# Optimization experiments

Measured on AMD Instinct MI355X. Metric: run time of the kernel, lower is better.

## Reference

```python
import jax, jax.numpy as jnp
import numpy as np

T = 5          # temporal_window_size
B = 512        # batch (graphs per timestep)
NA = 16        # num_agents (nodes per graph)
S = 64         # num_belief_states
A = 16         # action_dim
HID = 64       # hidden_dim per head
H = 4          # num_attn_heads
FD = HID * H   # 256, feature_dim
LAT = 128      # latent_dim
N = B * NA     # total nodes per timestep
FIN = S + A    # node feature dim
NEG_SLOPE = 0.2


def _edge_index():
    i, j = np.meshgrid(np.arange(NA), np.arange(NA), indexing='ij')
    m = i != j
    src_l, dst_l = i[m], j[m]                      # 240 intra-clique edges
    off = (np.arange(B) * NA)[:, None]
    src = (src_l[None] + off).ravel()
    dst = (dst_l[None] + off).ravel()
    loops = np.arange(N)                           # PyG GATConv add_self_loops=True
    src = np.concatenate([src, loops])
    dst = np.concatenate([dst, loops])
    return jnp.asarray(np.stack([src, dst]), dtype=jnp.int64)


def setup_inputs() -> dict:
    key = jax.random.key(0)
    ks = jax.random.split(key, 24)
    xav = lambda k, shp: jax.random.normal(k, shp, jnp.float32) * np.float32(np.sqrt(2.0 / (shp[0] + shp[-1])))
    return {
        'signals': jax.random.normal(ks[0], (T, B, S), jnp.float32),
        'neighbor_actions': jax.random.normal(ks[1], (T, B, NA * A), jnp.float32),
        'lin_w0': xav(ks[2], (FD, FIN)),
        'att_src0': xav(ks[3], (H, HID)),
        'att_dst0': xav(ks[4], (H, HID)),
        'bias0': jnp.zeros((FD,), jnp.float32),
        'lin_w1': xav(ks[5], (FD, FD)),
        'att_src1': xav(ks[6], (H, HID)),
        'att_dst1': xav(ks[7], (H, HID)),
        'bias1': jnp.zeros((FD,), jnp.float32),
        'in_proj_w': xav(ks[8], (3 * FD, FD)),
        'in_proj_b': jnp.zeros((3 * FD,), jnp.float32),
        'out_proj_w': xav(ks[9], (FD, FD)),
        'out_proj_b': jnp.zeros((FD,), jnp.float32),
        'w_mean': xav(ks[10], (LAT, FD)),
        'b_mean': jnp.zeros((LAT,), jnp.float32),
        'w_logvar': xav(ks[11], (LAT, FD)),
        'b_logvar': jnp.zeros((LAT,), jnp.float32),
        'w_belief': xav(ks[12], (S, FD)),
        'b_belief': jnp.zeros((S,), jnp.float32),
        'edge_index': _edge_index(),
    }


def _segment_softmax(e, seg, num_segments):
    # e: [E, T, H]; softmax over edges sharing the same target node.
    m = jax.ops.segment_max(e, seg, num_segments=num_segments)
    e = jnp.exp(e - m[seg])
    s = jax.ops.segment_sum(e, seg, num_segments=num_segments)
    return e / s[seg]


def _gat(x, src, dst, w, a_src, a_dst, b):
    # x: [N, T, Fin] -> [N, T, H*HID]   (PyG GATConv, concat heads)
    xl = jnp.einsum('ntf,of->nto', x, w).reshape(N, T, H, HID)
    e_src = jnp.einsum('nthc,hc->nth', xl, a_src)[src]   # [E, T, H]
    e_dst = jnp.einsum('nthc,hc->nth', xl, a_dst)[dst]
    e = jax.nn.leaky_relu(e_src + e_dst, NEG_SLOPE)
    alpha = _segment_softmax(e, dst, N)                  # per-target softmax
    out = jax.ops.segment_sum(alpha[..., None] * xl[src], dst, num_segments=N)
    return out.reshape(N, T, FD) + b


def reference(signals, neighbor_actions, lin_w0, att_src0, att_dst0, bias0,
              lin_w1, att_src1, att_dst1, bias1, in_proj_w, in_proj_b,
              out_proj_w, out_proj_b, w_mean, b_mean, w_logvar, b_logvar,
              w_belief, b_belief, edge_index):
    # --- _construct_graph (vectorized over time window + batch) ---
    acts = neighbor_actions.reshape(T, B, NA, A)
    beliefs = jnp.zeros((T, B, NA, S), signals.dtype).at[:, :, 0, :].set(signals)
    nodes = jnp.concatenate([beliefs, acts], -1).reshape(T, N, FIN)
    nodes = jnp.transpose(nodes, (1, 0, 2))              # [N, T, FIN]
    src, dst = edge_index[0], edge_index[1]
    x = jax.nn.relu(_gat(nodes, src, dst, lin_w0, att_src0, att_dst0, bias0))
    x = jax.nn.relu(_gat(x, src, dst, lin_w1, att_src1, att_dst1, bias1))
    # --- ego-node sequence: nodes 0, NA, 2*NA, ... ---
    seq = x[::NA]                                        # [B, T, FD]
    # --- temporal MultiheadAttention (batch_first, eval) ---
    qkv = seq @ in_proj_w.T + in_proj_b
    q, k, v = jnp.split(qkv, 3, axis=-1)
    dh = FD // H
    q = q.reshape(B, T, H, dh); k = k.reshape(B, T, H, dh); v = v.reshape(B, T, H, dh)
    scores = jnp.einsum('bqhd,bkhd->bhqk', q, k) / jnp.sqrt(jnp.asarray(dh, seq.dtype))
    # torch float attn_mask is ADDITIVE: mask[i,j]=1 if j<=i else 0
    mask = (jnp.arange(T)[:, None] >= jnp.arange(T)[None, :]).astype(seq.dtype)
    attn = jax.nn.softmax(scores + mask[None, None], axis=-1)
    ctx = jnp.einsum('bhqk,bkhd->bqhd', attn, v).reshape(B, T, FD)
    ctx = ctx @ out_proj_w.T + out_proj_b
    feat = ctx[:, -1]                                    # [B, FD]
    # --- heads ---
    mean = feat @ w_mean.T + b_mean
    logvar = feat @ w_logvar.T + b_logvar
    belief = jax.nn.softmax(feat @ w_belief.T + b_belief, axis=-1)
    return (mean, logvar, belief)
```

## Files before the change

### kernel.cpp

```cpp
#include <hip/hip_runtime.h>
#include <hip/hip_bf16.h>


__device__ __forceinline__ float wave_sum64(float v) {
    #pragma unroll
    for (int off = 32; off > 0; off >>= 1) v += __shfl_xor(v, off, 64);
    return v;
}
__device__ __forceinline__ float wave_max64(float v) {
    #pragma unroll
    for (int off = 32; off > 0; off >>= 1) v = fmaxf(v, __shfl_xor(v, off, 64));
    return v;
}

__global__ __launch_bounds__(256) void k_pre(
    const float* __restrict__ w0, const float* __restrict__ w1,
    const float* __restrict__ wip, const float* __restrict__ wop,
    const float* __restrict__ wm, const float* __restrict__ wlv,
    const float* __restrict__ wb,
    const float* __restrict__ as0, const float* __restrict__ ad0,
    const float* __restrict__ as1, const float* __restrict__ ad1,
    float* __restrict__ tws,
    float* __restrict__ u1, float* __restrict__ ud1,
    float* __restrict__ pa0, float* __restrict__ pd0)
{
    const int tid = threadIdx.x;
    if (blockIdx.x < 1680) {
        int i = blockIdx.x * 256 + tid;
        float v;
        if (i < 16384) {
            int k = i >> 8, n = i & 255;
            v = w0[n * 80 + k];
        } else if (i < 20480) {
            int j = i - 16384; int k = j >> 8, n = j & 255;
            v = w0[n * 80 + 64 + k];
        } else if (i < 86016) {
            int j = i - 20480; int k = j >> 8, n = j & 255;
            v = w1[n * 256 + k];
        } else if (i < 282624) {
            int j = i - 86016; int k = j / 768, n = j - k * 768;
            v = wip[n * 256 + k];
        } else if (i < 348160) {
            int j = i - 282624; int k = j >> 8, n = j & 255;
            v = wop[n * 256 + k];
        } else {
            int j = i - 348160; int k = j / 320, o = j - k * 320;
            if (o < 128)      v = wm[o * 256 + k];
            else if (o < 256) v = wlv[(o - 128) * 256 + k];
            else              v = wb[(o - 256) * 256 + k];
        }
        tws[i] = v;
        return;
    }
    for (int q = 0; q < 4; q++) {
        int idx = q * 256 + tid;
        int h = idx >> 8, k = idx & 255;
        float su = 0.f, sd = 0.f;
        for (int c = 0; c < 64; c++) {
            float wv = w1[(h * 64 + c) * 256 + k];
            su = fmaf(as1[h * 64 + c], wv, su);
            sd = fmaf(ad1[h * 64 + c], wv, sd);
        }
        u1[idx] = su; ud1[idx] = sd;
    }
    if (tid < 64) {
        int h = tid >> 4, k = tid & 15;
        float su = 0.f, sd = 0.f;
        for (int c = 0; c < 64; c++) {
            float wv = w0[(h * 64 + c) * 80 + 64 + k];
            su = fmaf(as0[h * 64 + c], wv, su);
            sd = fmaf(ad0[h * 64 + c], wv, sd);
        }
        pa0[tid] = su; pd0[tid] = sd;
    }
}

__global__ __launch_bounds__(256) void k_gat(
    const float* __restrict__ sig,
    const float* __restrict__ nact,
    const float* __restrict__ W0sT,
    const float* __restrict__ W0aT,
    const float* __restrict__ W1T,
    const float* __restrict__ u1g, const float* __restrict__ ud1g,
    const float* __restrict__ pa0g, const float* __restrict__ pd0g,
    const float* __restrict__ as0, const float* __restrict__ ad0,
    const float* __restrict__ b0, const float* __restrict__ b1,
    float* __restrict__ seqf)
{
    __shared__ float sigL[5][64];
    __shared__ float actL[5][16][16];
    __shared__ float SL[5][258];
    __shared__ float u1L[4][256], ud1L[4][256];
    __shared__ float pa0L[64], pd0L[64];
    __shared__ float sSL[5][4], dSL[5][4];
    __shared__ float es0L[5][16][4], ed0L[5][16][4];
    __shared__ float a0g[4][16][16];
    __shared__ float dL[4][16][16];
    __shared__ float x1L[16][258];
    __shared__ float espL[16][4][4];
    __shared__ float edpL[4][4];
    __shared__ float es1L[16][4];
    __shared__ float edL[4];
    __shared__ float alpha1L[4][16];
    __shared__ float zL[5][4][258];

    const int tid = threadIdx.x;
    const int b = blockIdx.x;

    for (int i = tid; i < 320; i += 256)
        sigL[i >> 6][i & 63] = sig[((i >> 6) * 512 + b) * 64 + (i & 63)];
    for (int i = tid; i < 1280; i += 256) {
        int g = i >> 8, r = i & 255;
        actL[g][r >> 4][r & 15] = nact[(g * 512 + b) * 256 + r];
    }
    for (int q = 0; q < 4; q++) {
        int idx = q * 256 + tid;
        u1L[idx >> 8][idx & 255] = u1g[idx];
        ud1L[idx >> 8][idx & 255] = ud1g[idx];
    }
    if (tid < 64) { pa0L[tid] = pa0g[tid]; pd0L[tid] = pd0g[tid]; }
    __syncthreads();

    {
        const int n = tid;
        float acc[5] = {0, 0, 0, 0, 0};
        for (int k = 0; k < 64; k++) {
            float wv = W0sT[k * 256 + n];
            #pragma unroll
            for (int g = 0; g < 5; g++) acc[g] = fmaf(sigL[g][k], wv, acc[g]);
        }
        #pragma unroll
        for (int g = 0; g < 5; g++) SL[g][n] = acc[g];
    }
    __syncthreads();

    if (tid < 20) {
        int g = tid / 4, h = tid & 3;
        float su = 0.f, sd = 0.f;
        for (int c = 0; c < 64; c++) {
            float sv = SL[g][h * 64 + c];
            su = fmaf(sv, as0[h * 64 + c], su);
            sd = fmaf(sv, ad0[h * 64 + c], sd);
        }
        sSL[g][h] = su; dSL[g][h] = sd;
    }
    __syncthreads();

    for (int q = tid; q < 320; q += 256) {
        int g = q >> 6, r = q & 63, m = r >> 2, h = r & 3;
        float su = (m == 0) ? sSL[g][h] : 0.f;
        float sd = (m == 0) ? dSL[g][h] : 0.f;
        #pragma unroll
        for (int k = 0; k < 16; k++) {
            float av = actL[g][m][k];
            su = fmaf(av, pa0L[h * 16 + k], su);
            sd = fmaf(av, pd0L[h * 16 + k], sd);
        }
        es0L[g][m][h] = su; ed0L[g][m][h] = sd;
    }
    __syncthreads();

    for (int g = 0; g < 5; g++) {
        if (tid < 64) {
            int h = tid >> 4, j = tid & 15;
            float ej = ed0L[g][j][h];
            float e[16], m = -1e30f;
            #pragma unroll
            for (int s = 0; s < 16; s++) {
                float x = es0L[g][s][h] + ej;
                x = (x >= 0.f) ? x : 0.2f * x;
                e[s] = x; m = fmaxf(m, x);
            }
            float sum = 0.f;
            #pragma unroll
            for (int s = 0; s < 16; s++) { e[s] = __expf(e[s] - m); sum += e[s]; }
            float inv = 1.f / sum;
            #pragma unroll
            for (int s = 0; s < 16; s++) a0g[h][j][s] = e[s] * inv;
        }
        __syncthreads();

        #pragma unroll
        for (int q = 0; q < 4; q++) {
            int idx = q * 256 + tid;
            int h = idx >> 8, j = (idx >> 4) & 15, k = idx & 15;
            float a = 0.f;
            #pragma unroll
            for (int s = 0; s < 16; s++)
                a = fmaf(a0g[h][j][s], actL[g][s][k], a);
            dL[h][j][k] = a;
        }
        __syncthreads();

        {
            const int n = tid, h = n >> 6;
            float sv = SL[g][n], b0v = b0[n];
            float accj[16];
            #pragma unroll
            for (int j = 0; j < 16; j++)
                accj[j] = fmaf(a0g[h][j][0], sv, b0v);
            #pragma unroll
            for (int k = 0; k < 16; k++) {
                float wv = W0aT[k * 256 + n];
                #pragma unroll
                for (int j = 0; j < 16; j++)
                    accj[j] = fmaf(dL[h][j][k], wv, accj[j]);
            }
            #pragma unroll
            for (int j = 0; j < 16; j++)
                x1L[j][n] = fmaxf(accj[j], 0.f);
        }
        __syncthreads();

        {
            int m = tid >> 4, h = (tid >> 2) & 3, p = tid & 3;
            float a = 0.f;
            for (int kk = 0; kk < 64; kk++) {
                int k = kk * 4 + p;
                a = fmaf(x1L[m][k], u1L[h][k], a);
            }
            espL[m][h][p] = a;
            if (m == 0) {
                float ad = 0.f;
                for (int kk = 0; kk < 64; kk++) {
                    int k = kk * 4 + p;
                    ad = fmaf(x1L[0][k], ud1L[h][k], ad);
                }
                edpL[h][p] = ad;
            }
        }
        __syncthreads();
        if (tid < 64) {
            int m = tid >> 2, h = tid & 3;
            es1L[m][h] = espL[m][h][0] + espL[m][h][1] + espL[m][h][2] + espL[m][h][3];
        }
        if (tid < 4)
            edL[tid] = edpL[tid][0] + edpL[tid][1] + edpL[tid][2] + edpL[tid][3];
        __syncthreads();

        if (tid < 4) {
            int h = tid;
            float ej = edL[h];
            float e[16], m = -1e30f;
            #pragma unroll
            for (int s = 0; s < 16; s++) {
                float x = es1L[s][h] + ej;
                x = (x >= 0.f) ? x : 0.2f * x;
                e[s] = x; m = fmaxf(m, x);
            }
            float sum = 0.f;
            #pragma unroll
            for (int s = 0; s < 16; s++) { e[s] = __expf(e[s] - m); sum += e[s]; }
            float inv = 1.f / sum;
            #pragma unroll
            for (int s = 0; s < 16; s++) alpha1L[h][s] = e[s] * inv;
        }
        __syncthreads();

        {
            const int k = tid;
            float xv[16];
            #pragma unroll
            for (int s = 0; s < 16; s++) xv[s] = x1L[s][k];
            #pragma unroll
            for (int h = 0; h < 4; h++) {
                float zv = 0.f;
                #pragma unroll
                for (int s = 0; s < 16; s++)
                    zv = fmaf(alpha1L[h][s], xv[s], zv);
                zL[g][h][k] = zv;
            }
        }
        __syncthreads();
    }

    {
        const int n = tid, h = n >> 6;
        float b1v = b1[n];
        float acc[5] = {b1v, b1v, b1v, b1v, b1v};
        for (int k = 0; k < 256; k++) {
            float wv = W1T[k * 256 + n];
            #pragma unroll
            for (int g = 0; g < 5; g++)
                acc[g] = fmaf(zL[g][h][k], wv, acc[g]);
        }
        #pragma unroll
        for (int g = 0; g < 5; g++)
            seqf[(b * 5 + g) * 256 + n] = fmaxf(acc[g], 0.f);
    }
}

__global__ __launch_bounds__(768) void k_stage2(
    const float* __restrict__ seqf,
    const float* __restrict__ wipT,
    const float* __restrict__ bip,
    const float* __restrict__ wopT,
    const float* __restrict__ bop,
    const float* __restrict__ whT,
    const float* __restrict__ bm, const float* __restrict__ blv,
    const float* __restrict__ bb,
    float* __restrict__ out)
{
    __shared__ float sseq[2][5][256];
    __shared__ float kL[2][5][256], vL[2][5][256], qL[2][256];
    __shared__ float ctxL[2][256], featL[2][256];
    __shared__ float beliefL[2][64];
    const int tid = threadIdx.x;
    const int b0 = blockIdx.x * 2;

    {
        float* sflat = &sseq[0][0][0];
        for (int i = tid; i < 2560; i += 768)
            sflat[i] = seqf[b0 * 1280 + i];
    }
    __syncthreads();

    {
        const int kind = tid >> 8, n = tid & 255;
        if (kind == 0) {
            float a0 = 0.f, a1 = 0.f;
            for (int k = 0; k < 256; k++) {
                float wv = wipT[k * 768 + n];
                a0 = fmaf(sseq[0][4][k], wv, a0);
                a1 = fmaf(sseq[1][4][k], wv, a1);
            }
            float bv = bip[n];
            qL[0][n] = a0 + bv; qL[1][n] = a1 + bv;
        } else {
            const float* wcol = wipT + kind * 256 + n;
            float acc[2][5];
            #pragma unroll
            for (int gb = 0; gb < 2; gb++)
                #pragma unroll
                for (int t = 0; t < 5; t++) acc[gb][t] = 0.f;
            for (int k = 0; k < 256; k++) {
                float wv = wcol[k * 768];
                #pragma unroll
                for (int gb = 0; gb < 2; gb++) {
                    #pragma unroll
                    for (int t = 0; t < 5; t++)
                        acc[gb][t] = fmaf(sseq[gb][t][k], wv, acc[gb][t]);
                }
            }
            float bv = bip[kind * 256 + n];
            float* dst = (kind == 1) ? &kL[0][0][0] : &vL[0][0][0];
            #pragma unroll
            for (int gb = 0; gb < 2; gb++)
                #pragma unroll
                for (int t = 0; t < 5; t++)
                    dst[gb * 1280 + t * 256 + n] = acc[gb][t] + bv;
        }
    }
    __syncthreads();

    if (tid < 512) {
        const int gb = tid >> 8, col = tid & 255;
        float q4 = qL[gb][col];
        float sc[5];
        #pragma unroll
        for (int t = 0; t < 5; t++)
            sc[t] = wave_sum64(q4 * kL[gb][t][col]) * 0.125f;
        float m = sc[0];
        #pragma unroll
        for (int t = 1; t < 5; t++) m = fmaxf(m, sc[t]);
        float p[5], sum = 0.f;
        #pragma unroll
        for (int t = 0; t < 5; t++) { p[t] = __expf(sc[t] - m); sum += p[t]; }
        float inv = 1.f / sum, cv = 0.f;
        #pragma unroll
        for (int t = 0; t < 5; t++) cv = fmaf(p[t], vL[gb][t][col], cv);
        ctxL[gb][col] = cv * inv;
    }
    __syncthreads();

    if (tid < 512) {
        const int gb = tid >> 8, n = tid & 255;
        float acc = 0.f;
        for (int k = 0; k < 256; k++)
            acc = fmaf(ctxL[gb][k], wopT[k * 256 + n], acc);
        featL[gb][n] = acc + bop[n];
    }
    __syncthreads();

    if (tid < 640) {
        const int gb = tid / 320, j = tid - gb * 320;
        float acc = 0.f;
        for (int k = 0; k < 256; k++)
            acc = fmaf(featL[gb][k], whT[k * 320 + j], acc);
        if (j < 128) {
            out[(b0 + gb) * 128 + j] = acc + bm[j];
        } else if (j < 256) {
            out[65536 + (b0 + gb) * 128 + (j - 128)] = acc + blv[j - 128];
        } else {
            beliefL[gb][j - 256] = acc + bb[j - 256];
        }
    }
    __syncthreads();

    if (tid < 128) {
        int gb = tid >> 6, lane = tid & 63;
        float lg = beliefL[gb][lane];
        float m = wave_max64(lg);
        float e = __expf(lg - m);
        float s = wave_sum64(e);
        out[131072 + (b0 + gb) * 64 + lane] = e / s;
    }
}

extern "C" void kernel_launch(void* const* d_in, const int* in_sizes, int n_in,
                              void* d_out, int out_size, void* d_ws, size_t ws_size,
                              hipStream_t stream) {
    const float* sig  = (const float*)d_in[0];
    const float* nact = (const float*)d_in[1];
    const float* w0   = (const float*)d_in[2];
    const float* as0  = (const float*)d_in[3];
    const float* ad0  = (const float*)d_in[4];
    const float* b0   = (const float*)d_in[5];
    const float* w1   = (const float*)d_in[6];
    const float* as1  = (const float*)d_in[7];
    const float* ad1  = (const float*)d_in[8];
    const float* b1   = (const float*)d_in[9];
    const float* wip  = (const float*)d_in[10];
    const float* bip  = (const float*)d_in[11];
    const float* wop  = (const float*)d_in[12];
    const float* bop  = (const float*)d_in[13];
    const float* wm   = (const float*)d_in[14];
    const float* bm   = (const float*)d_in[15];
    const float* wlv  = (const float*)d_in[16];
    const float* blv  = (const float*)d_in[17];
    const float* wb   = (const float*)d_in[18];
    const float* bb   = (const float*)d_in[19];

    float* ws    = (float*)d_ws;
    float* seqf  = ws;
    float* tws   = ws + 655360;
    float* W0sT  = tws;
    float* W0aT  = tws + 16384;
    float* W1T   = tws + 20480;
    float* wipT  = tws + 86016;
    float* wopT  = tws + 282624;
    float* whT   = tws + 348160;
    float* u1    = ws + 1085440;
    float* ud1   = ws + 1086464;
    float* pa0   = ws + 1087488;
    float* pd0   = ws + 1087552;

    k_pre   <<<1681, 256, 0, stream>>>(w0, w1, wip, wop, wm, wlv, wb,
                                       as0, ad0, as1, ad1,
                                       tws, u1, ud1, pa0, pd0);
    k_gat   <<<512, 256, 0, stream>>>(sig, nact, W0sT, W0aT, W1T,
                                      u1, ud1, pa0, pd0, as0, ad0, b0, b1, seqf);
    k_stage2<<<256, 768, 0, stream>>>(seqf, wipT, bip, wopT, bop, whT,
                                      bm, blv, bb, (float*)d_out);
}
```

Measured before the change: 205.2 us.

## Fuse GAT and temporal-attention stages into one kernel per graph

Merges the GAT kernel and the temporal attention/heads kernel into a single kernel, one block per graph, so the per-graph sequence features stay in shared memory instead of round-tripping through a global workspace. Shared memory is packed into one manually laid out buffer that reuses dead GAT regions for the q/k/v and context buffers, and the u1/ud1 rows are padded. This removes one launch and the seqf global write and read. In exchange, stage-2 weight reads are no longer shared across two graphs per block, and each block now streams the full QKV weight matrix alone with only 256 threads.

Result: slower. 211.7 us (+3.2%).

```diff
diff --git a/kernel.cpp b/kernel.cpp
--- a/kernel.cpp
+++ b/kernel.cpp
@@ -75,223 +75,15 @@
     }
 }
 
-__global__ __launch_bounds__(256) void k_gat(
+__global__ __launch_bounds__(256) void k_fused(
     const float* __restrict__ sig,
     const float* __restrict__ nact,
-    const float* __restrict__ W0sT,
-    const float* __restrict__ W0aT,
+    const float* __restrict__ W0sT, const float* __restrict__ W0aT,
     const float* __restrict__ W1T,
     const float* __restrict__ u1g, const float* __restrict__ ud1g,
     const float* __restrict__ pa0g, const float* __restrict__ pd0g,
     const float* __restrict__ as0, const float* __restrict__ ad0,
     const float* __restrict__ b0, const float* __restrict__ b1,
-    float* __restrict__ seqf)
-{
-    __shared__ float sigL[5][64];
-    __shared__ float actL[5][16][16];
-    __shared__ float SL[5][258];
-    __shared__ float u1L[4][256], ud1L[4][256];
-    __shared__ float pa0L[64], pd0L[64];
-    __shared__ float sSL[5][4], dSL[5][4];
-    __shared__ float es0L[5][16][4], ed0L[5][16][4];
-    __shared__ float a0g[4][16][16];
-    __shared__ float dL[4][16][16];
-    __shared__ float x1L[16][258];
-    __shared__ float espL[16][4][4];
-    __shared__ float edpL[4][4];
-    __shared__ float es1L[16][4];
-    __shared__ float edL[4];
-    __shared__ float alpha1L[4][16];
-    __shared__ float zL[5][4][258];
-
-    const int tid = threadIdx.x;
-    const int b = blockIdx.x;
-
-    for (int i = tid; i < 320; i += 256)
-        sigL[i >> 6][i & 63] = sig[((i >> 6) * 512 + b) * 64 + (i & 63)];
-    for (int i = tid; i < 1280; i += 256) {
-        int g = i >> 8, r = i & 255;
-        actL[g][r >> 4][r & 15] = nact[(g * 512 + b) * 256 + r];
-    }
-    for (int q = 0; q < 4; q++) {
-        int idx = q * 256 + tid;
-        u1L[idx >> 8][idx & 255] = u1g[idx];
-        ud1L[idx >> 8][idx & 255] = ud1g[idx];
-    }
-    if (tid < 64) { pa0L[tid] = pa0g[tid]; pd0L[tid] = pd0g[tid]; }
-    __syncthreads();
-
-    {
-        const int n = tid;
-        float acc[5] = {0, 0, 0, 0, 0};
-        for (int k = 0; k < 64; k++) {
-            float wv = W0sT[k * 256 + n];
-            #pragma unroll
-            for (int g = 0; g < 5; g++) acc[g] = fmaf(sigL[g][k], wv, acc[g]);
-        }
-        #pragma unroll
-        for (int g = 0; g < 5; g++) SL[g][n] = acc[g];
-    }
-    __syncthreads();
-
-    if (tid < 20) {
-        int g = tid / 4, h = tid & 3;
-        float su = 0.f, sd = 0.f;
-        for (int c = 0; c < 64; c++) {
-            float sv = SL[g][h * 64 + c];
-            su = fmaf(sv, as0[h * 64 + c], su);
-            sd = fmaf(sv, ad0[h * 64 + c], sd);
-        }
-        sSL[g][h] = su; dSL[g][h] = sd;
-    }
-    __syncthreads();
-
-    for (int q = tid; q < 320; q += 256) {
-        int g = q >> 6, r = q & 63, m = r >> 2, h = r & 3;
-        float su = (m == 0) ? sSL[g][h] : 0.f;
-        float sd = (m == 0) ? dSL[g][h] : 0.f;
-        #pragma unroll
-        for (int k = 0; k < 16; k++) {
-            float av = actL[g][m][k];
-            su = fmaf(av, pa0L[h * 16 + k], su);
-            sd = fmaf(av, pd0L[h * 16 + k], sd);
-        }
-        es0L[g][m][h] = su; ed0L[g][m][h] = sd;
-    }
-    __syncthreads();
-
-    for (int g = 0; g < 5; g++) {
-        if (tid < 64) {
-            int h = tid >> 4, j = tid & 15;
-            float ej = ed0L[g][j][h];
-            float e[16], m = -1e30f;
-            #pragma unroll
-            for (int s = 0; s < 16; s++) {
-                float x = es0L[g][s][h] + ej;
-                x = (x >= 0.f) ? x : 0.2f * x;
-                e[s] = x; m = fmaxf(m, x);
-            }
-            float sum = 0.f;
-            #pragma unroll
-            for (int s = 0; s < 16; s++) { e[s] = __expf(e[s] - m); sum += e[s]; }
-            float inv = 1.f / sum;
-            #pragma unroll
-            for (int s = 0; s < 16; s++) a0g[h][j][s] = e[s] * inv;
-        }
-        __syncthreads();
-
-        #pragma unroll
-        for (int q = 0; q < 4; q++) {
-            int idx = q * 256 + tid;
-            int h = idx >> 8, j = (idx >> 4) & 15, k = idx & 15;
-            float a = 0.f;
-            #pragma unroll
-            for (int s = 0; s < 16; s++)
-                a = fmaf(a0g[h][j][s], actL[g][s][k], a);
-            dL[h][j][k] = a;
-        }
-        __syncthreads();
-
-        {
-            const int n = tid, h = n >> 6;
-            float sv = SL[g][n], b0v = b0[n];
-            float accj[16];
-            #pragma unroll
-            for (int j = 0; j < 16; j++)
-                accj[j] = fmaf(a0g[h][j][0], sv, b0v);
-            #pragma unroll
-            for (int k = 0; k < 16; k++) {
-                float wv = W0aT[k * 256 + n];
-                #pragma unroll
-                for (int j = 0; j < 16; j++)
-                    accj[j] = fmaf(dL[h][j][k], wv, accj[j]);
-            }
-            #pragma unroll
-            for (int j = 0; j < 16; j++)
-                x1L[j][n] = fmaxf(accj[j], 0.f);
-        }
-        __syncthreads();
-
-        {
-            int m = tid >> 4, h = (tid >> 2) & 3, p = tid & 3;
-            float a = 0.f;
-            for (int kk = 0; kk < 64; kk++) {
-                int k = kk * 4 + p;
-                a = fmaf(x1L[m][k], u1L[h][k], a);
-            }
-            espL[m][h][p] = a;
-            if (m == 0) {
-                float ad = 0.f;
-                for (int kk = 0; kk < 64; kk++) {
-                    int k = kk * 4 + p;
-                    ad = fmaf(x1L[0][k], ud1L[h][k], ad);
-                }
-                edpL[h][p] = ad;
-            }
-        }
-        __syncthreads();
-        if (tid < 64) {
-            int m = tid >> 2, h = tid & 3;
-            es1L[m][h] = espL[m][h][0] + espL[m][h][1] + espL[m][h][2] + espL[m][h][3];
-        }
-        if (tid < 4)
-            edL[tid] = edpL[tid][0] + edpL[tid][1] + edpL[tid][2] + edpL[tid][3];
-        __syncthreads();
-
-        if (tid < 4) {
-            int h = tid;
-            float ej = edL[h];
-            float e[16], m = -1e30f;
-            #pragma unroll
-            for (int s = 0; s < 16; s++) {
-                float x = es1L[s][h] + ej;
-                x = (x >= 0.f) ? x : 0.2f * x;
-                e[s] = x; m = fmaxf(m, x);
-            }
-            float sum = 0.f;
-            #pragma unroll
-            for (int s = 0; s < 16; s++) { e[s] = __expf(e[s] - m); sum += e[s]; }
-            float inv = 1.f / sum;
-            #pragma unroll
-            for (int s = 0; s < 16; s++) alpha1L[h][s] = e[s] * inv;
-        }
-        __syncthreads();
-
-        {
-            const int k = tid;
-            float xv[16];
-            #pragma unroll
-            for (int s = 0; s < 16; s++) xv[s] = x1L[s][k];
-            #pragma unroll
-            for (int h = 0; h < 4; h++) {
-                float zv = 0.f;
-                #pragma unroll
-                for (int s = 0; s < 16; s++)
-                    zv = fmaf(alpha1L[h][s], xv[s], zv);
-                zL[g][h][k] = zv;
-            }
-        }
-        __syncthreads();
-    }
-
-    {
-        const int n = tid, h = n >> 6;
-        float b1v = b1[n];
-        float acc[5] = {b1v, b1v, b1v, b1v, b1v};
-        for (int k = 0; k < 256; k++) {
-            float wv = W1T[k * 256 + n];
-            #pragma unroll
-            for (int g = 0; g < 5; g++)
-                acc[g] = fmaf(zL[g][h][k], wv, acc[g]);
-        }
-        #pragma unroll
-        for (int g = 0; g < 5; g++)
-            seqf[(b * 5 + g) * 256 + n] = fmaxf(acc[g], 0.f);
-    }
-}
-
-__global__ __launch_bounds__(768) void k_stage2(
-    const float* __restrict__ seqf,
     const float* __restrict__ wipT,
     const float* __restrict__ bip,
     const float* __restrict__ wopT,
@@ -301,65 +93,254 @@
     const float* __restrict__ bb,
     float* __restrict__ out)
 {
-    __shared__ float sseq[2][5][256];
-    __shared__ float kL[2][5][256], vL[2][5][256], qL[2][256];
-    __shared__ float ctxL[2][256], featL[2][256];
-    __shared__ float beliefL[2][64];
+    __shared__ __align__(16) char smem[75232];
+    float* sigL   = (float*)(smem + 0);
+    float* actL   = (float*)(smem + 1280);
+    float* SL     = (float*)(smem + 6400);
+    float* u1L    = (float*)(smem + 11560);
+    float* ud1L   = (float*)(smem + 15720);
+    float* pa0L   = (float*)(smem + 19880);
+    float* pd0L   = (float*)(smem + 20136);
+    float* sSL    = (float*)(smem + 20392);
+    float* dSL    = (float*)(smem + 20472);
+    float* es0L   = (float*)(smem + 20552);
+    float* ed0L   = (float*)(smem + 21832);
+    float* a0g    = (float*)(smem + 23112);
+    float* dL     = (float*)(smem + 27208);
+    float* x1L    = (float*)(smem + 31304);
+    float* espL   = (float*)(smem + 47816);
+    float* edpL   = (float*)(smem + 48840);
+    float* es1L   = (float*)(smem + 48904);
+    float* edL    = (float*)(smem + 49160);
+    float* alpha1L= (float*)(smem + 49176);
+    float* zL     = (float*)(smem + 49432);
+    float* sseq   = (float*)(smem + 70072);
+    float* kLp    = (float*)(smem + 11560);
+    float* vLp    = (float*)(smem + 16680);
+    float* qLp    = (float*)(smem + 23112);
+    float* ctxLp  = (float*)(smem + 24136);
+    float* featLp = (float*)(smem + 25160);
+    float* belLp  = (float*)(smem + 27208);
+
     const int tid = threadIdx.x;
-    const int b0 = blockIdx.x * 2;
+    const int b = blockIdx.x;
+
+    for (int i = tid; i < 320; i += 256)
+        sigL[i] = sig[((i >> 6) * 512 + b) * 64 + (i & 63)];
+    for (int i = tid; i < 1280; i += 256)
+        actL[i] = nact[((i >> 8) * 512 + b) * 256 + (i & 255)];
+    #pragma unroll
+    for (int q = 0; q < 4; q++) {
+        int idx = q * 256 + tid;
+        int h = idx >> 8, k = idx & 255;
+        u1L[h * 260 + k] = u1g[idx];
+        ud1L[h * 260 + k] = ud1g[idx];
+    }
+    if (tid < 64) { pa0L[tid] = pa0g[tid]; pd0L[tid] = pd0g[tid]; }
+    __syncthreads();
 
     {
-        float* sflat = &sseq[0][0][0];
-        for (int i = tid; i < 2560; i += 768)
-            sflat[i] = seqf[b0 * 1280 + i];
-    }
-    __syncthreads();
+        const int n = tid;
+        float acc[5] = {0, 0, 0, 0, 0};
+        for (int k = 0; k < 64; k++) {
+            float wv = W0sT[k * 256 + n];
+            #pragma unroll
+            for (int g = 0; g < 5; g++) acc[g] = fmaf(sigL[g * 64 + k], wv, acc[g]);
+        }
+        #pragma unroll
+        for (int g = 0; g < 5; g++) SL[g * 258 + n] = acc[g];
+    }
+    __syncthreads();
+
+    if (tid < 20) {
+        int g = tid / 4, h = tid & 3;
+        float su = 0.f, sd = 0.f;
+        for (int c = 0; c < 64; c++) {
+            float sv = SL[g * 258 + h * 64 + c];
+            su = fmaf(sv, as0[h * 64 + c], su);
+            sd = fmaf(sv, ad0[h * 64 + c], sd);
+        }
+        sSL[g * 4 + h] = su; dSL[g * 4 + h] = sd;
+    }
+    __syncthreads();
+
+    for (int q = tid; q < 320; q += 256) {
+        int g = q >> 6, r = q & 63, m = r >> 2, h = r & 3;
+        float su = (m == 0) ? sSL[g * 4 + h] : 0.f;
+        float sd = (m == 0) ? dSL[g * 4 + h] : 0.f;
+        #pragma unroll
+        for (int k = 0; k < 16; k++) {
+            float av = actL[g * 256 + m * 16 + k];
+            su = fmaf(av, pa0L[h * 16 + k], su);
+            sd = fmaf(av, pd0L[h * 16 + k], sd);
+        }
+        es0L[g * 64 + m * 4 + h] = su; ed0L[g * 64 + m * 4 + h] = sd;
+    }
+    __syncthreads();
+
+    for (int g = 0; g < 5; g++) {
+        if (tid < 64) {
+            int h = tid >> 4, j = tid & 15;
+            float ej = ed0L[g * 64 + j * 4 + h];
+            float e[16], m = -1e30f;
+            #pragma unroll
+            for (int s = 0; s < 16; s++) {
+                float x = es0L[g * 64 + s * 4 + h] + ej;
+                x = (x >= 0.f) ? x : 0.2f * x;
+                e[s] = x; m = fmaxf(m, x);
+            }
+            float sum = 0.f;
+            #pragma unroll
+            for (int s = 0; s < 16; s++) { e[s] = __expf(e[s] - m); sum += e[s]; }
+            float inv = 1.f / sum;
+            #pragma unroll
+            for (int s = 0; s < 16; s++) a0g[h * 256 + j * 16 + s] = e[s] * inv;
+        }
+        __syncthreads();
+
+        #pragma unroll
+        for (int q = 0; q < 4; q++) {
+            int idx = q * 256 + tid;
+            int h = idx >> 8, j = (idx >> 4) & 15, k = idx & 15;
+            float a = 0.f;
+            #pragma unroll
+            for (int s = 0; s < 16; s++)
+                a = fmaf(a0g[h * 256 + j * 16 + s], actL[g * 256 + s * 16 + k], a);
+            dL[h * 256 + j * 16 + k] = a;
+        }
+        __syncthreads();
+
+        {
+            const int n = tid, h = n >> 6;
+            float sv = SL[g * 258 + n], b0v = b0[n];
+            float accj[16];
+            #pragma unroll
+            for (int j = 0; j < 16; j++)
+                accj[j] = fmaf(a0g[h * 256 + j * 16], sv, b0v);
+            #pragma unroll
+            for (int k = 0; k < 16; k++) {
+                float wv = W0aT[k * 256 + n];
+                #pragma unroll
+                for (int j = 0; j < 16; j++)
+                    accj[j] = fmaf(dL[h * 256 + j * 16 + k], wv, accj[j]);
+            }
+            #pragma unroll
+            for (int j = 0; j < 16; j++)
+                x1L[j * 258 + n] = fmaxf(accj[j], 0.f);
+        }
+        __syncthreads();
+
+        {
+            int m = tid >> 4, h = (tid >> 2) & 3, p = tid & 3;
+            float a = 0.f;
+            for (int kk = 0; kk < 64; kk++) {
+                int k = kk * 4 + p;
+                a = fmaf(x1L[m * 258 + k], u1L[h * 260 + k], a);
+            }
+            espL[m * 16 + h * 4 + p] = a;
+            if (m == 0) {
+                float ad = 0.f;
+                for (int kk = 0; kk < 64; kk++) {
+                    int k = kk * 4 + p;
+                    ad = fmaf(x1L[k], ud1L[h * 260 + k], ad);
+                }
+                edpL[h * 4 + p] = ad;
+            }
+        }
+        __syncthreads();
+        if (tid < 64) {
+            int m = tid >> 2, h = tid & 3;
+            const float* e = espL + m * 16 + h * 4;
+            es1L[m * 4 + h] = e[0] + e[1] + e[2] + e[3];
+        }
+        if (tid < 4)
+            edL[tid] = edpL[tid * 4] + edpL[tid * 4 + 1] + edpL[tid * 4 + 2] + edpL[tid * 4 + 3];
+        __syncthreads();
+
+        if (tid < 4) {
+            int h = tid;
+            float ej = edL[h];
+            float e[16], m = -1e30f;
+            #pragma unroll
+            for (int s = 0; s < 16; s++) {
+                float x = es1L[s * 4 + h] + ej;
+                x = (x >= 0.f) ? x : 0.2f * x;
+                e[s] = x; m = fmaxf(m, x);
+            }
+            float sum = 0.f;
+            #pragma unroll
+            for (int s = 0; s < 16; s++) { e[s] = __expf(e[s] - m); sum += e[s]; }
+            float inv = 1.f / sum;
+            #pragma unroll
+            for (int s = 0; s < 16; s++) alpha1L[h * 16 + s] = e[s] * inv;
+        }
+        __syncthreads();
+
+        {
+            const int k = tid;
+            float xv[16];
+            #pragma unroll
+            for (int s = 0; s < 16; s++) xv[s] = x1L[s * 258 + k];
+            #pragma unroll
+            for (int h = 0; h < 4; h++) {
+                float zv = 0.f;
+                #pragma unroll
+                for (int s = 0; s < 16; s++)
+                    zv = fmaf(alpha1L[h * 16 + s], xv[s], zv);
+                zL[g * 1032 + h * 258 + k] = zv;
+            }
+        }
+        __syncthreads();
+    }
 
     {
-        const int kind = tid >> 8, n = tid & 255;
-        if (kind == 0) {
-            float a0 = 0.f, a1 = 0.f;
-            for (int k = 0; k < 256; k++) {
-                float wv = wipT[k * 768 + n];
-                a0 = fmaf(sseq[0][4][k], wv, a0);
-                a1 = fmaf(sseq[1][4][k], wv, a1);
-            }
-            float bv = bip[n];
-            qL[0][n] = a0 + bv; qL[1][n] = a1 + bv;
-        } else {
-            const float* wcol = wipT + kind * 256 + n;
-            float acc[2][5];
-            #pragma unroll
-            for (int gb = 0; gb < 2; gb++)
-                #pragma unroll
-                for (int t = 0; t < 5; t++) acc[gb][t] = 0.f;
-            for (int k = 0; k < 256; k++) {
-                float wv = wcol[k * 768];
-                #pragma unroll
-                for (int gb = 0; gb < 2; gb++) {
-                    #pragma unroll
-                    for (int t = 0; t < 5; t++)
-                        acc[gb][t] = fmaf(sseq[gb][t][k], wv, acc[gb][t]);
-                }
-            }
-            float bv = bip[kind * 256 + n];
-            float* dst = (kind == 1) ? &kL[0][0][0] : &vL[0][0][0];
-            #pragma unroll
-            for (int gb = 0; gb < 2; gb++)
-                #pragma unroll
-                for (int t = 0; t < 5; t++)
-                    dst[gb * 1280 + t * 256 + n] = acc[gb][t] + bv;
-        }
-    }
-    __syncthreads();
-
-    if (tid < 512) {
-        const int gb = tid >> 8, col = tid & 255;
-        float q4 = qL[gb][col];
+        const int n = tid, h = n >> 6;
+        float b1v = b1[n];
+        float acc[5] = {b1v, b1v, b1v, b1v, b1v};
+        for (int k = 0; k < 256; k++) {
+            float wv = W1T[k * 256 + n];
+            #pragma unroll
+            for (int g = 0; g < 5; g++)
+                acc[g] = fmaf(zL[g * 1032 + h * 258 + k], wv, acc[g]);
+        }
+        #pragma unroll
+        for (int g = 0; g < 5; g++)
+            sseq[g * 258 + n] = fmaxf(acc[g], 0.f);
+    }
+    __syncthreads();
+
+    {
+        const int n = tid;
+        float accq = 0.f, acck[5] = {0, 0, 0, 0, 0}, accv[5] = {0, 0, 0, 0, 0};
+        for (int k = 0; k < 256; k++) {
+            float wq = wipT[k * 768 + n];
+            float wk = wipT[k * 768 + 256 + n];
+            float wv = wipT[k * 768 + 512 + n];
+            accq = fmaf(sseq[4 * 258 + k], wq, accq);
+            #pragma unroll
+            for (int t = 0; t < 5; t++) {
+                float sv = sseq[t * 258 + k];
+                acck[t] = fmaf(sv, wk, acck[t]);
+                accv[t] = fmaf(sv, wv, accv[t]);
+            }
+        }
+        qLp[n] = accq + bip[n];
+        float bk = bip[256 + n], bv = bip[512 + n];
+        #pragma unroll
+        for (int t = 0; t < 5; t++) {
+            kLp[t * 256 + n] = acck[t] + bk;
+            vLp[t * 256 + n] = accv[t] + bv;
+        }
+    }
+    __syncthreads();
+
+    {
+        const int col = tid;
+        float q4 = qLp[col];
         float sc[5];
         #pragma unroll
         for (int t = 0; t < 5; t++)
-            sc[t] = wave_sum64(q4 * kL[gb][t][col]) * 0.125f;
+            sc[t] = wave_sum64(q4 * kLp[t * 256 + col]) * 0.125f;
         float m = sc[0];
         #pragma unroll
         for (int t = 1; t < 5; t++) m = fmaxf(m, sc[t]);
@@ -368,42 +349,36 @@
         for (int t = 0; t < 5; t++) { p[t] = __expf(sc[t] - m); sum += p[t]; }
         float inv = 1.f / sum, cv = 0.f;
         #pragma unroll
-        for (int t = 0; t < 5; t++) cv = fmaf(p[t], vL[gb][t][col], cv);
-        ctxL[gb][col] = cv * inv;
-    }
-    __syncthreads();
-
-    if (tid < 512) {
-        const int gb = tid >> 8, n = tid & 255;
+        for (int t = 0; t < 5; t++) cv = fmaf(p[t], vLp[t * 256 + col], cv);
+        ctxLp[col] = cv * inv;
+    }
+    __syncthreads();
+
+    {
+        const int n = tid;
         float acc = 0.f;
         for (int k = 0; k < 256; k++)
-            acc = fmaf(ctxL[gb][k], wopT[k * 256 + n], acc);
-        featL[gb][n] = acc + bop[n];
-    }
-    __syncthreads();
-
-    if (tid < 640) {
-        const int gb = tid / 320, j = tid - gb * 320;
+            acc = fmaf(ctxLp[k], wopT[k * 256 + n], acc);
+        featLp[n] = acc + bop[n];
+    }
+    __syncthreads();
+
+    for (int j = tid; j < 320; j += 256) {
         float acc = 0.f;
         for (int k = 0; k < 256; k++)
-            acc = fmaf(featL[gb][k], whT[k * 320 + j], acc);
-        if (j < 128) {
-            out[(b0 + gb) * 128 + j] = acc + bm[j];
-        } else if (j < 256) {
-            out[65536 + (b0 + gb) * 128 + (j - 128)] = acc + blv[j - 128];
-        } else {
-            beliefL[gb][j - 256] = acc + bb[j - 256];
-        }
-    }
-    __syncthreads();
-
-    if (tid < 128) {
-        int gb = tid >> 6, lane = tid & 63;
-        float lg = beliefL[gb][lane];
+            acc = fmaf(featLp[k], whT[k * 320 + j], acc);
+        if (j < 128)       out[b * 128 + j] = acc + bm[j];
+        else if (j < 256)  out[65536 + b * 128 + (j - 128)] = acc + blv[j - 128];
+        else               belLp[j - 256] = acc + bb[j - 256];
+    }
+    __syncthreads();
+
+    if (tid < 64) {
+        float lg = belLp[tid];
         float m = wave_max64(lg);
         float e = __expf(lg - m);
         float s = wave_sum64(e);
-        out[131072 + (b0 + gb) * 64 + lane] = e / s;
+        out[131072 + b * 64 + tid] = e / s;
     }
 }
 
@@ -432,24 +407,23 @@
     const float* bb   = (const float*)d_in[19];
 
     float* ws    = (float*)d_ws;
-    float* seqf  = ws;
-    float* tws   = ws + 655360;
+    float* tws   = ws;
     float* W0sT  = tws;
     float* W0aT  = tws + 16384;
     float* W1T   = tws + 20480;
     float* wipT  = tws + 86016;
     float* wopT  = tws + 282624;
     float* whT   = tws + 348160;
-    float* u1    = ws + 1085440;
-    float* ud1   = ws + 1086464;
-    float* pa0   = ws + 1087488;
-    float* pd0   = ws + 1087552;
-
-    k_pre   <<<1681, 256, 0, stream>>>(w0, w1, wip, wop, wm, wlv, wb,
-                                       as0, ad0, as1, ad1,
-                                       tws, u1, ud1, pa0, pd0);
-    k_gat   <<<512, 256, 0, stream>>>(sig, nact, W0sT, W0aT, W1T,
-                                      u1, ud1, pa0, pd0, as0, ad0, b0, b1, seqf);
-    k_stage2<<<256, 768, 0, stream>>>(seqf, wipT, bip, wopT, bop, whT,
-                                      bm, blv, bb, (float*)d_out);
+    float* u1    = ws + 430080;
+    float* ud1   = ws + 431104;
+    float* pa0   = ws + 432128;
+    float* pd0   = ws + 432192;
+
+    k_pre  <<<1681, 256, 0, stream>>>(w0, w1, wip, wop, wm, wlv, wb,
+                                      as0, ad0, as1, ad1,
+                                      tws, u1, ud1, pa0, pd0);
+    k_fused<<<512, 256, 0, stream>>>(sig, nact, W0sT, W0aT, W1T,
+                                     u1, ud1, pa0, pd0, as0, ad0, b0, b1,
+                                     wipT, bip, wopT, bop, whT, bm, blv, bb,
+                                     (float*)d_out);
 }
```

## Split GAT kernel across timesteps: one block per (batch, timestep) pair

Applied to the files above, without the earlier changes.

The GAT kernel previously ran 512 blocks, each looping serially over the 5 timesteps. It now launches 2560 blocks, one per (batch, timestep), and packs shared memory into a single aliased buffer padded to 257. This cuts shared memory per block and raises occupancy and parallelism on the GPU. In exchange, the W0sT and W1T weight rows are reread per timestep rather than reused across 5 accumulators in registers, so global and L2 weight traffic rises.

Measured after the change: 204.6 us. Within noise of the previous version (-0.3%).

```diff
diff --git a/kernel.cpp b/kernel.cpp
--- a/kernel.cpp
+++ b/kernel.cpp
@@ -87,206 +87,189 @@
     const float* __restrict__ b0, const float* __restrict__ b1,
     float* __restrict__ seqf)
 {
-    __shared__ float sigL[5][64];
-    __shared__ float actL[5][16][16];
-    __shared__ float SL[5][258];
-    __shared__ float u1L[4][256], ud1L[4][256];
-    __shared__ float pa0L[64], pd0L[64];
-    __shared__ float sSL[5][4], dSL[5][4];
-    __shared__ float es0L[5][16][4], ed0L[5][16][4];
-    __shared__ float a0g[4][16][16];
-    __shared__ float dL[4][16][16];
-    __shared__ float x1L[16][258];
-    __shared__ float espL[16][4][4];
-    __shared__ float edpL[4][4];
-    __shared__ float es1L[16][4];
-    __shared__ float edL[4];
-    __shared__ float alpha1L[4][16];
-    __shared__ float zL[5][4][258];
+    __shared__ __align__(16) char smem[36832];
+    float* actL   = (float*)(smem + 0);
+    float* u1L    = (float*)(smem + 1024);
+    float* ud1L   = (float*)(smem + 5136);
+    float* pa0L   = (float*)(smem + 9248);
+    float* pd0L   = (float*)(smem + 9504);
+    float* sSL    = (float*)(smem + 9760);
+    float* dSL    = (float*)(smem + 9776);
+    float* es0L   = (float*)(smem + 9792);
+    float* ed0L   = (float*)(smem + 10048);
+    float* a0L    = (float*)(smem + 10304);
+    float* dLa    = (float*)(smem + 14400);
+    float* zLa    = (float*)(smem + 14400);
+    float* x1L    = (float*)(smem + 18512);
+    float* espL   = (float*)(smem + 34960);
+    float* edpL   = (float*)(smem + 35984);
+    float* es1L   = (float*)(smem + 36048);
+    float* edLx   = (float*)(smem + 36304);
+    float* alpha1L= (float*)(smem + 36320);
+    float* sigL   = (float*)(smem + 36576);
 
     const int tid = threadIdx.x;
-    const int b = blockIdx.x;
-
-    for (int i = tid; i < 320; i += 256)
-        sigL[i >> 6][i & 63] = sig[((i >> 6) * 512 + b) * 64 + (i & 63)];
-    for (int i = tid; i < 1280; i += 256) {
-        int g = i >> 8, r = i & 255;
-        actL[g][r >> 4][r & 15] = nact[(g * 512 + b) * 256 + r];
-    }
+    const int bg = blockIdx.x;
+    const int b = bg / 5, g = bg - b * 5;
+    const int n = tid, w = tid >> 6, lane = tid & 63;
+
+    if (tid < 64) sigL[tid] = sig[(g * 512 + b) * 64 + tid];
+    actL[tid] = nact[(g * 512 + b) * 256 + tid];
+    #pragma unroll
     for (int q = 0; q < 4; q++) {
         int idx = q * 256 + tid;
-        u1L[idx >> 8][idx & 255] = u1g[idx];
-        ud1L[idx >> 8][idx & 255] = ud1g[idx];
-    }
-    if (tid < 64) { pa0L[tid] = pa0g[tid]; pd0L[tid] = pd0g[tid]; }
-    __syncthreads();
-
-    {
-        const int n = tid;
-        float acc[5] = {0, 0, 0, 0, 0};
-        for (int k = 0; k < 64; k++) {
-            float wv = W0sT[k * 256 + n];
-            #pragma unroll
-            for (int g = 0; g < 5; g++) acc[g] = fmaf(sigL[g][k], wv, acc[g]);
-        }
-        #pragma unroll
-        for (int g = 0; g < 5; g++) SL[g][n] = acc[g];
-    }
-    __syncthreads();
-
-    if (tid < 20) {
-        int g = tid / 4, h = tid & 3;
-        float su = 0.f, sd = 0.f;
-        for (int c = 0; c < 64; c++) {
-            float sv = SL[g][h * 64 + c];
-            su = fmaf(sv, as0[h * 64 + c], su);
-            sd = fmaf(sv, ad0[h * 64 + c], sd);
-        }
-        sSL[g][h] = su; dSL[g][h] = sd;
-    }
-    __syncthreads();
-
-    for (int q = tid; q < 320; q += 256) {
-        int g = q >> 6, r = q & 63, m = r >> 2, h = r & 3;
-        float su = (m == 0) ? sSL[g][h] : 0.f;
-        float sd = (m == 0) ? dSL[g][h] : 0.f;
+        int h = idx >> 8, k = idx & 255;
+        u1L[h * 257 + k] = u1g[idx];
+        ud1L[h * 257 + k] = ud1g[idx];
+    }
+    if (tid >= 64 && tid < 128) { pa0L[tid - 64] = pa0g[tid - 64]; pd0L[tid - 64] = pd0g[tid - 64]; }
+    __syncthreads();
+
+    float S = 0.f;
+    for (int k = 0; k < 64; k++)
+        S = fmaf(sigL[k], W0sT[k * 256 + n], S);
+    {
+        float ps = wave_sum64(S * as0[n]);
+        float pd_ = wave_sum64(S * ad0[n]);
+        if (lane == 0) { sSL[w] = ps; dSL[w] = pd_; }
+    }
+    __syncthreads();
+
+    if (tid < 64) {
+        int m = tid >> 2, h = tid & 3;
+        float su = (m == 0) ? sSL[h] : 0.f;
+        float sd = (m == 0) ? dSL[h] : 0.f;
         #pragma unroll
         for (int k = 0; k < 16; k++) {
-            float av = actL[g][m][k];
+            float av = actL[m * 16 + k];
             su = fmaf(av, pa0L[h * 16 + k], su);
             sd = fmaf(av, pd0L[h * 16 + k], sd);
         }
-        es0L[g][m][h] = su; ed0L[g][m][h] = sd;
-    }
-    __syncthreads();
-
-    for (int g = 0; g < 5; g++) {
-        if (tid < 64) {
-            int h = tid >> 4, j = tid & 15;
-            float ej = ed0L[g][j][h];
-            float e[16], m = -1e30f;
+        es0L[m * 4 + h] = su; ed0L[m * 4 + h] = sd;
+    }
+    __syncthreads();
+
+    if (tid < 64) {
+        int h = tid >> 4, j = tid & 15;
+        float ej = ed0L[j * 4 + h];
+        float e[16], m = -1e30f;
+        #pragma unroll
+        for (int s = 0; s < 16; s++) {
+            float x = es0L[s * 4 + h] + ej;
+            x = (x >= 0.f) ? x : 0.2f * x;
+            e[s] = x; m = fmaxf(m, x);
+        }
+        float sum = 0.f;
+        #pragma unroll
+        for (int s = 0; s < 16; s++) { e[s] = __expf(e[s] - m); sum += e[s]; }
+        float inv = 1.f / sum;
+        #pragma unroll
+        for (int s = 0; s < 16; s++) a0L[h * 256 + j * 16 + s] = e[s] * inv;
+    }
+    __syncthreads();
+
+    #pragma unroll
+    for (int q = 0; q < 4; q++) {
+        int idx = q * 256 + tid;
+        int h = idx >> 8, j = (idx >> 4) & 15, k = idx & 15;
+        float a = 0.f;
+        #pragma unroll
+        for (int s = 0; s < 16; s++)
+            a = fmaf(a0L[h * 256 + j * 16 + s], actL[s * 16 + k], a);
+        dLa[h * 256 + j * 16 + k] = a;
+    }
+    __syncthreads();
+
+    float x1r[16];
+    {
+        const int h = w;
+        float b0v = b0[n];
+        #pragma unroll
+        for (int j = 0; j < 16; j++)
+            x1r[j] = fmaf(a0L[h * 256 + j * 16], S, b0v);
+        #pragma unroll
+        for (int k = 0; k < 16; k++) {
+            float wv = W0aT[k * 256 + n];
             #pragma unroll
-            for (int s = 0; s < 16; s++) {
-                float x = es0L[g][s][h] + ej;
-                x = (x >= 0.f) ? x : 0.2f * x;
-                e[s] = x; m = fmaxf(m, x);
+            for (int j = 0; j < 16; j++)
+                x1r[j] = fmaf(dLa[h * 256 + j * 16 + k], wv, x1r[j]);
+        }
+        #pragma unroll
+        for (int j = 0; j < 16; j++) {
+            x1r[j] = fmaxf(x1r[j], 0.f);
+            x1L[j * 257 + n] = x1r[j];
+        }
+    }
+    __syncthreads();
+
+    {
+        int m = tid >> 4, h = (tid >> 2) & 3, p = tid & 3;
+        float a = 0.f;
+        for (int kk = 0; kk < 64; kk++) {
+            int k = kk * 4 + p;
+            a = fmaf(x1L[m * 257 + k], u1L[h * 257 + k], a);
+        }
+        espL[m * 16 + h * 4 + p] = a;
+        if (m == 0) {
+            float ad = 0.f;
+            for (int kk = 0; kk < 64; kk++) {
+                int k = kk * 4 + p;
+                ad = fmaf(x1L[k], ud1L[h * 257 + k], ad);
             }
-            float sum = 0.f;
-            #pragma unroll
-            for (int s = 0; s < 16; s++) { e[s] = __expf(e[s] - m); sum += e[s]; }
-            float inv = 1.f / sum;
-            #pragma unroll
-            for (int s = 0; s < 16; s++) a0g[h][j][s] = e[s] * inv;
-        }
-        __syncthreads();
-
-        #pragma unroll
-        for (int q = 0; q < 4; q++) {
-            int idx = q * 256 + tid;
-            int h = idx >> 8, j = (idx >> 4) & 15, k = idx & 15;
-            float a = 0.f;
+            edpL[h * 4 + p] = ad;
+        }
+    }
+    __syncthreads();
+    if (tid < 64) {
+        int m = tid >> 2, h = tid & 3;
+        const float* e = espL + m * 16 + h * 4;
+        es1L[m * 4 + h] = e[0] + e[1] + e[2] + e[3];
+    }
+    if (tid < 4)
+        edLx[tid] = edpL[tid * 4] + edpL[tid * 4 + 1] + edpL[tid * 4 + 2] + edpL[tid * 4 + 3];
+    __syncthreads();
+
+    if (tid < 4) {
+        int h = tid;
+        float ej = edLx[h];
+        float e[16], m = -1e30f;
+        #pragma unroll
+        for (int s = 0; s < 16; s++) {
+            float x = es1L[s * 4 + h] + ej;
+            x = (x >= 0.f) ? x : 0.2f * x;
+            e[s] = x; m = fmaxf(m, x);
+        }
+        float sum = 0.f;
+        #pragma unroll
+        for (int s = 0; s < 16; s++) { e[s] = __expf(e[s] - m); sum += e[s]; }
+        float inv = 1.f / sum;
+        #pragma unroll
+        for (int s = 0; s < 16; s++) alpha1L[h * 16 + s] = e[s] * inv;
+    }
+    __syncthreads();
+
+    {
+        const int k = tid;
+        float xv[16];
+        #pragma unroll
+        for (int s = 0; s < 16; s++) xv[s] = x1L[s * 257 + k];
+        #pragma unroll
+        for (int h = 0; h < 4; h++) {
+            float zv = 0.f;
             #pragma unroll
             for (int s = 0; s < 16; s++)
-                a = fmaf(a0g[h][j][s], actL[g][s][k], a);
-            dL[h][j][k] = a;
-        }
-        __syncthreads();
-
-        {
-            const int n = tid, h = n >> 6;
-            float sv = SL[g][n], b0v = b0[n];
-            float accj[16];
-            #pragma unroll
-            for (int j = 0; j < 16; j++)
-                accj[j] = fmaf(a0g[h][j][0], sv, b0v);
-            #pragma unroll
-            for (int k = 0; k < 16; k++) {
-                float wv = W0aT[k * 256 + n];
-                #pragma unroll
-                for (int j = 0; j < 16; j++)
-                    accj[j] = fmaf(dL[h][j][k], wv, accj[j]);
-            }
-            #pragma unroll
-            for (int j = 0; j < 16; j++)
-                x1L[j][n] = fmaxf(accj[j], 0.f);
-        }
-        __syncthreads();
-
-        {
-            int m = tid >> 4, h = (tid >> 2) & 3, p = tid & 3;
-            float a = 0.f;
-            for (int kk = 0; kk < 64; kk++) {
-                int k = kk * 4 + p;
-                a = fmaf(x1L[m][k], u1L[h][k], a);
-            }
-            espL[m][h][p] = a;
-            if (m == 0) {
-                float ad = 0.f;
-                for (int kk = 0; kk < 64; kk++) {
-                    int k = kk * 4 + p;
-                    ad = fmaf(x1L[0][k], ud1L[h][k], ad);
-                }
-                edpL[h][p] = ad;
-            }
-        }
-        __syncthreads();
-        if (tid < 64) {
-            int m = tid >> 2, h = tid & 3;
-            es1L[m][h] = espL[m][h][0] + espL[m][h][1] + espL[m][h][2] + espL[m][h][3];
-        }
-        if (tid < 4)
-            edL[tid] = edpL[tid][0] + edpL[tid][1] + edpL[tid][2] + edpL[tid][3];
-        __syncthreads();
-
-        if (tid < 4) {
-            int h = tid;
-            float ej = edL[h];
-            float e[16], m = -1e30f;
-            #pragma unroll
-            for (int s = 0; s < 16; s++) {
-                float x = es1L[s][h] + ej;
-                x = (x >= 0.f) ? x : 0.2f * x;
-                e[s] = x; m = fmaxf(m, x);
-            }
-            float sum = 0.f;
-            #pragma unroll
-            for (int s = 0; s < 16; s++) { e[s] = __expf(e[s] - m); sum += e[s]; }
-            float inv = 1.f / sum;
-            #pragma unroll
-            for (int s = 0; s < 16; s++) alpha1L[h][s] = e[s] * inv;
-        }
-        __syncthreads();
-
-        {
-            const int k = tid;
-            float xv[16];
-            #pragma unroll
-            for (int s = 0; s < 16; s++) xv[s] = x1L[s][k];
-            #pragma unroll
-            for (int h = 0; h < 4; h++) {
-                float zv = 0.f;
-                #pragma unroll
-                for (int s = 0; s < 16; s++)
-                    zv = fmaf(alpha1L[h][s], xv[s], zv);
-                zL[g][h][k] = zv;
-            }
-        }
-        __syncthreads();
-    }
-
-    {
-        const int n = tid, h = n >> 6;
-        float b1v = b1[n];
-        float acc[5] = {b1v, b1v, b1v, b1v, b1v};
-        for (int k = 0; k < 256; k++) {
-            float wv = W1T[k * 256 + n];
-            #pragma unroll
-            for (int g = 0; g < 5; g++)
-                acc[g] = fmaf(zL[g][h][k], wv, acc[g]);
-        }
-        #pragma unroll
-        for (int g = 0; g < 5; g++)
-            seqf[(b * 5 + g) * 256 + n] = fmaxf(acc[g], 0.f);
+                zv = fmaf(alpha1L[h * 16 + s], xv[s], zv);
+            zLa[h * 257 + k] = zv;
+        }
+    }
+    __syncthreads();
+
+    {
+        const int h = w;
+        float acc = b1[n];
+        for (int k = 0; k < 256; k++)
+            acc = fmaf(zLa[h * 257 + k], W1T[k * 256 + n], acc);
+        seqf[bg * 256 + n] = fmaxf(acc, 0.f);
     }
 }
 
@@ -448,8 +431,8 @@
     k_pre   <<<1681, 256, 0, stream>>>(w0, w1, wip, wop, wm, wlv, wb,
                                        as0, ad0, as1, ad1,
                                        tws, u1, ud1, pa0, pd0);
-    k_gat   <<<512, 256, 0, stream>>>(sig, nact, W0sT, W0aT, W1T,
-                                      u1, ud1, pa0, pd0, as0, ad0, b0, b1, seqf);
+    k_gat   <<<2560, 256, 0, stream>>>(sig, nact, W0sT, W0aT, W1T,
+                                       u1, ud1, pa0, pd0, as0, ad0, b0, b1, seqf);
     k_stage2<<<256, 768, 0, stream>>>(seqf, wipT, bip, wopT, bop, whT,
                                       bm, blv, bb, (float*)d_out);
 }
```
